# Performance work log

Hardware: AMD Instinct MI355X
Metric: run time of the kernel (lower is better)

The kernel has to match this reference:

```python
import jax, jax.numpy as jnp
import numpy as np

PNUM = 128
BATCH = 8192


def setup_inputs() -> dict:
    key = jax.random.key(0)
    k0, k1, k2 = jax.random.split(key, 3)
    return {
        "pred0": jax.random.normal(k0, (BATCH, PNUM, 2), dtype=jnp.float32),
        "pred1": jax.random.normal(k1, (BATCH, PNUM, 2), dtype=jnp.float32),
        "gt": jax.random.normal(k2, (BATCH, PNUM, 2), dtype=jnp.float32),
    }


def _smooth_l1(d):
    # F.smooth_l1_loss with default beta=1.0, reduction='none'
    a = jnp.abs(d)
    return jnp.where(a < 1.0, 0.5 * d * d, a - 0.5)


def _match_loss(pred, gt):
    # pred, gt: [B, pnum, 2]
    pnum = pred.shape[1]
    # cyclic index: idx[i, j] = (i + j) % pnum  (row i = gt rolled by i)
    idx = (jnp.arange(pnum)[:, None] + jnp.arange(pnum)[None, :]) % pnum
    gt_expand = gt[:, idx]                      # [B, pnum, pnum, 2]
    diff = pred[:, None, :, :] - gt_expand      # broadcast pred over shift dim i
    dis = _smooth_l1(diff).sum(-1).mean(axis=2)  # [B, pnum] mean over vertices j
    return jnp.min(dis, axis=1)                  # min over cyclic shift i -> [B]


def reference(pred0, pred1, gt):
    loss = _match_loss(pred0, gt).mean() + _match_loss(pred1, gt).mean()
    return loss / 2.0
```

## Files before the change

### kernel.cpp

```cpp
#include <hip/hip_runtime.h>
#include <stdint.h>

#define PNUM 128
#define BATCH 8192
#define WPB 4
#define GRID1 (BATCH / WPB)

typedef uint32_t u32;
typedef uint32_t u32x2 __attribute__((ext_vector_type(2)));
typedef uint32_t u32x4 __attribute__((ext_vector_type(4)));

__device__ __forceinline__ u32 cvt2u(float x, float y) {
    return __builtin_bit_cast(u32, __builtin_amdgcn_cvt_pkrtz(x, y));
}

#define DSR64(dst, addr) \
    asm volatile("ds_read_b64 %0, %1" : "=v"(dst) : "v"(addr))
#define DSR128(dst, addr, OFF) \
    asm volatile("ds_read_b128 %0, %1 offset:" OFF : "=v"(dst) : "v"(addr))
#define DSR2x64(dst, addr) \
    asm volatile("ds_read2_b64 %0, %1 offset0:1 offset1:2" : "=v"(dst) : "v"(addr))
#define WAITLG(N) \
    asm volatile("s_waitcnt lgkmcnt(" #N ")" ::: "memory"); \
    __builtin_amdgcn_sched_barrier(0)

#define QUAD(p0,q0,A0, p1,q1,A1, p2,q2,A2, p3,q3,A3) do { \
    u32 d0_, d1_, d2_, d3_, m0_, m1_, m2_, m3_, t0_, t1_, t2_, t3_; \
    asm volatile("v_pk_add_f16 %0, %1, %2 neg_lo:[0,1] neg_hi:[0,1]" : "=v"(d0_) : "v"(p0), "v"(q0)); \
    asm volatile("v_pk_add_f16 %0, %1, %2 neg_lo:[0,1] neg_hi:[0,1]" : "=v"(d1_) : "v"(p1), "v"(q1)); \
    asm volatile("v_pk_add_f16 %0, %1, %2 neg_lo:[0,1] neg_hi:[0,1]" : "=v"(d2_) : "v"(p2), "v"(q2)); \
    asm volatile("v_pk_add_f16 %0, %1, %2 neg_lo:[0,1] neg_hi:[0,1]" : "=v"(d3_) : "v"(p3), "v"(q3)); \
    asm volatile("v_and_b32 %0, 0x7fff7fff, %0" : "+v"(d0_)); \
    asm volatile("v_and_b32 %0, 0x7fff7fff, %0" : "+v"(d1_)); \
    asm volatile("v_and_b32 %0, 0x7fff7fff, %0" : "+v"(d2_)); \
    asm volatile("v_and_b32 %0, 0x7fff7fff, %0" : "+v"(d3_)); \
    asm volatile("v_pk_min_f16 %0, %1, %2" : "=v"(m0_) : "v"(d0_), "v"(cOne)); \
    asm volatile("v_pk_min_f16 %0, %1, %2" : "=v"(m1_) : "v"(d1_), "v"(cOne)); \
    asm volatile("v_pk_min_f16 %0, %1, %2" : "=v"(m2_) : "v"(d2_), "v"(cOne)); \
    asm volatile("v_pk_min_f16 %0, %1, %2" : "=v"(m3_) : "v"(d3_), "v"(cOne)); \
    asm volatile("v_pk_fma_f16 %0, %1, %2, %3" : "=v"(t0_) : "v"(m0_), "v"(cNegHalf), "v"(d0_)); \
    asm volatile("v_pk_fma_f16 %0, %1, %2, %3" : "=v"(t1_) : "v"(m1_), "v"(cNegHalf), "v"(d1_)); \
    asm volatile("v_pk_fma_f16 %0, %1, %2, %3" : "=v"(t2_) : "v"(m2_), "v"(cNegHalf), "v"(d2_)); \
    asm volatile("v_pk_fma_f16 %0, %1, %2, %3" : "=v"(t3_) : "v"(m3_), "v"(cNegHalf), "v"(d3_)); \
    asm volatile("v_dot2_f32_f16 %0, %1, %2, %0" : "+v"(A0) : "v"(m0_), "v"(t0_)); \
    asm volatile("v_dot2_f32_f16 %0, %1, %2, %0" : "+v"(A1) : "v"(m1_), "v"(t1_)); \
    asm volatile("v_dot2_f32_f16 %0, %1, %2, %0" : "+v"(A2) : "v"(m2_), "v"(t2_)); \
    asm volatile("v_dot2_f32_f16 %0, %1, %2, %0" : "+v"(A3) : "v"(m3_), "v"(t3_)); \
} while (0)

#define ISSUE(Bg, Bq0, Bq1) \
    DSR2x64(Bg, issGA); \
    DSR128(Bq0, issPA, "0"); \
    DSR128(Bq1, issPA, "512"); \
    issGA += 16; issPA += 16

#define COMPUTE(G, Q0, Q1, W0, W1, DO_ISSUE) \
    QUAD(Q0[0], W0,   a00,  Q0[0], W1,   a01,  Q1[0], W0,   a10,  Q1[0], W1,   a11); \
    DO_ISSUE; \
    QUAD(Q0[1], W1,   a00,  Q0[1], G[0], a01,  Q1[1], W1,   a10,  Q1[1], G[0], a11); \
    QUAD(Q0[2], G[0], a00,  Q0[2], G[1], a01,  Q1[2], G[0], a10,  Q1[2], G[1], a11); \
    QUAD(Q0[3], G[1], a00,  Q0[3], G[2], a01,  Q1[3], G[1], a10,  Q1[3], G[2], a11)

__global__ __launch_bounds__(64 * WPB, 8) void match_fused(
        const float* __restrict__ pred0,
        const float* __restrict__ pred1,
        const float* __restrict__ gt,
        float* __restrict__ ws) {
    __shared__ __align__(16) _Float16 lds[WPB][1024];
    __shared__ float bsum[WPB];

    const int t = threadIdx.x;
    const int k = t & 63;
    const int w = __builtin_amdgcn_readfirstlane(t >> 6);
    const int b = blockIdx.x * WPB + w;

    _Float16* base = lds[w];
    uint2* ringU = (uint2*)base;
    uint2* q0s   = (uint2*)(base + 512);
    uint2* q1s   = (uint2*)(base + 768);

    const float4* gv4 = (const float4*)(gt    + (size_t)b * (PNUM * 2));
    const float4* p0v = (const float4*)(pred0 + (size_t)b * (PNUM * 2));
    const float4* p1v = (const float4*)(pred1 + (size_t)b * (PNUM * 2));
    {
        float4 g = gv4[k];
        uint2 gh = {cvt2u(g.x, g.y), cvt2u(g.z, g.w)};
        ringU[k] = gh; ringU[k + 64] = gh;
        float4 p = p0v[k];
        q0s[k] = (uint2){cvt2u(p.x, p.y), cvt2u(p.z, p.w)};
        p = p1v[k];
        q1s[k] = (uint2){cvt2u(p.x, p.y), cvt2u(p.z, p.w)};
    }

    const u32 ldsb = (u32)(uintptr_t)base;
    u32 issGA = ldsb + (u32)(k * 8);
    u32 issPA = ldsb + 1024;

    asm volatile("s_waitcnt lgkmcnt(0)" ::: "memory");
    __builtin_amdgcn_sched_barrier(0);

    const u32 cOne = 0x3C003C00u;
    const u32 cNegHalf = 0xB800B800u;

    u32x2 Wsp;
    DSR64(Wsp, issGA);
    u32x4 b0g, b0q0, b0q1, b1g, b1q0, b1q1, b2g, b2q0, b2q1;
    ISSUE(b0g, b0q0, b0q1);
    ISSUE(b1g, b1q0, b1q1);

    float a00 = 0.f, a01 = 0.f, a10 = 0.f, a11 = 0.f;

    WAITLG(3); COMPUTE(b0g, b0q0, b0q1, Wsp[0], Wsp[1], ISSUE(b2g, b2q0, b2q1));
    WAITLG(3); COMPUTE(b1g, b1q0, b1q1, b0g[2], b0g[3], ISSUE(b0g, b0q0, b0q1));
    WAITLG(3); COMPUTE(b2g, b2q0, b2q1, b1g[2], b1g[3], ISSUE(b1g, b1q0, b1q1));

#pragma unroll 1
    for (int tr = 0; tr < 9; ++tr) {
        WAITLG(3); COMPUTE(b0g, b0q0, b0q1, b2g[2], b2g[3], ISSUE(b2g, b2q0, b2q1));
        WAITLG(3); COMPUTE(b1g, b1q0, b1q1, b0g[2], b0g[3], ISSUE(b0g, b0q0, b0q1));
        WAITLG(3); COMPUTE(b2g, b2q0, b2q1, b1g[2], b1g[3], ISSUE(b1g, b1q0, b1q1));
    }
    WAITLG(3); COMPUTE(b0g, b0q0, b0q1, b2g[2], b2g[3], );
    WAITLG(0); COMPUTE(b1g, b1q0, b1q1, b0g[2], b0g[3], );

    float r0 = fminf(a00, a01);
    float r1 = fminf(a10, a11);
#pragma unroll
    for (int m = 32; m > 0; m >>= 1) {
        r0 = fminf(r0, __shfl_xor(r0, m, 64));
        r1 = fminf(r1, __shfl_xor(r1, m, 64));
    }

    if (k == 0) bsum[w] = r0 + r1;
    __syncthreads();
    if (t == 0) {
        ws[blockIdx.x] = bsum[0] + bsum[1] + bsum[2] + bsum[3];
    }
}

__global__ __launch_bounds__(256) void reduce_out(
        const float* __restrict__ ws, float* __restrict__ out) {
    const int t = threadIdx.x;
    const float4* w4 = (const float4*)ws;
    float4 v0 = w4[t];
    float4 v1 = w4[t + 256];
    float s = ((v0.x + v0.y) + (v0.z + v0.w)) + ((v1.x + v1.y) + (v1.z + v1.w));
#pragma unroll
    for (int m = 32; m > 0; m >>= 1) s += __shfl_xor(s, m, 64);
    __shared__ float acc[4];
    const int w = t >> 6;
    if ((t & 63) == 0) acc[w] = s;
    __syncthreads();
    if (t == 0)
        out[0] = (acc[0] + acc[1] + acc[2] + acc[3]) * (1.0f / (2.0f * BATCH * PNUM));
}

extern "C" void kernel_launch(void* const* d_in, const int* in_sizes, int n_in,
                              void* d_out, int out_size, void* d_ws, size_t ws_size,
                              hipStream_t stream) {
    const float* pred0 = (const float*)d_in[0];
    const float* pred1 = (const float*)d_in[1];
    const float* gt    = (const float*)d_in[2];
    float* out = (float*)d_out;
    float* ws  = (float*)d_ws;

    match_fused<<<GRID1, 64 * WPB, 0, stream>>>(pred0, pred1, gt, ws);
    reduce_out<<<1, 256, 0, stream>>>(ws, out);
}
```

Before: 110.4 us.

## Fully unroll LDS-read pipeline with 4-deep ring and immediate offsets

Replaces the 3-buffer rolling loop (unroll 1) with a fully unrolled 32-step loop over a 4-slot register ring. LDS reads use constant immediate offsets instead of incremented address registers, and the prefetch distance grows from 2 to 3 steps, with waitcnt thresholds adjusted to match. The aim is to hide LDS latency better and drop loop and address overhead. In exchange, register pressure rises, so the occupancy hint in launch_bounds drops from 8 to 6.

```diff
diff --git a/kernel.cpp b/kernel.cpp
--- a/kernel.cpp
+++ b/kernel.cpp
@@ -13,16 +13,6 @@
 __device__ __forceinline__ u32 cvt2u(float x, float y) {
     return __builtin_bit_cast(u32, __builtin_amdgcn_cvt_pkrtz(x, y));
 }
-
-#define DSR64(dst, addr) \
-    asm volatile("ds_read_b64 %0, %1" : "=v"(dst) : "v"(addr))
-#define DSR128(dst, addr, OFF) \
-    asm volatile("ds_read_b128 %0, %1 offset:" OFF : "=v"(dst) : "v"(addr))
-#define DSR2x64(dst, addr) \
-    asm volatile("ds_read2_b64 %0, %1 offset0:1 offset1:2" : "=v"(dst) : "v"(addr))
-#define WAITLG(N) \
-    asm volatile("s_waitcnt lgkmcnt(" #N ")" ::: "memory"); \
-    __builtin_amdgcn_sched_barrier(0)
 
 #define QUAD(p0,q0,A0, p1,q1,A1, p2,q2,A2, p3,q3,A3) do { \
     u32 d0_, d1_, d2_, d3_, m0_, m1_, m2_, m3_, t0_, t1_, t2_, t3_; \
@@ -48,20 +38,7 @@
     asm volatile("v_dot2_f32_f16 %0, %1, %2, %0" : "+v"(A3) : "v"(m3_), "v"(t3_)); \
 } while (0)
 
-#define ISSUE(Bg, Bq0, Bq1) \
-    DSR2x64(Bg, issGA); \
-    DSR128(Bq0, issPA, "0"); \
-    DSR128(Bq1, issPA, "512"); \
-    issGA += 16; issPA += 16
-
-#define COMPUTE(G, Q0, Q1, W0, W1, DO_ISSUE) \
-    QUAD(Q0[0], W0,   a00,  Q0[0], W1,   a01,  Q1[0], W0,   a10,  Q1[0], W1,   a11); \
-    DO_ISSUE; \
-    QUAD(Q0[1], W1,   a00,  Q0[1], G[0], a01,  Q1[1], W1,   a10,  Q1[1], G[0], a11); \
-    QUAD(Q0[2], G[0], a00,  Q0[2], G[1], a01,  Q1[2], G[0], a10,  Q1[2], G[1], a11); \
-    QUAD(Q0[3], G[1], a00,  Q0[3], G[2], a01,  Q1[3], G[1], a10,  Q1[3], G[2], a11)
-
-__global__ __launch_bounds__(64 * WPB, 8) void match_fused(
+__global__ __launch_bounds__(64 * WPB, 6) void match_fused(
         const float* __restrict__ pred0,
         const float* __restrict__ pred1,
         const float* __restrict__ gt,
@@ -93,8 +70,8 @@
     }
 
     const u32 ldsb = (u32)(uintptr_t)base;
-    u32 issGA = ldsb + (u32)(k * 8);
-    u32 issPA = ldsb + 1024;
+    u32 gA = ldsb + (u32)(k * 8);
+    u32 pA = ldsb;
 
     asm volatile("s_waitcnt lgkmcnt(0)" ::: "memory");
     __builtin_amdgcn_sched_barrier(0);
@@ -103,25 +80,50 @@
     const u32 cNegHalf = 0xB800B800u;
 
     u32x2 Wsp;
-    DSR64(Wsp, issGA);
-    u32x4 b0g, b0q0, b0q1, b1g, b1q0, b1q1, b2g, b2q0, b2q1;
-    ISSUE(b0g, b0q0, b0q1);
-    ISSUE(b1g, b1q0, b1q1);
+    asm volatile("ds_read_b64 %0, %1" : "=v"(Wsp) : "v"(gA));
+    u32x4 G[4], Q0[4], Q1[4];
+#pragma unroll
+    for (int h = 0; h < 3; ++h) {
+        asm volatile("ds_read2_b64 %0, %1 offset0:%c2 offset1:%c3"
+                     : "=v"(G[h]) : "v"(gA), "i"(2 * h + 1), "i"(2 * h + 2));
+        asm volatile("ds_read_b128 %0, %1 offset:%c2"
+                     : "=v"(Q0[h]) : "v"(pA), "i"(1024 + 16 * h));
+        asm volatile("ds_read_b128 %0, %1 offset:%c2"
+                     : "=v"(Q1[h]) : "v"(pA), "i"(1536 + 16 * h));
+    }
 
     float a00 = 0.f, a01 = 0.f, a10 = 0.f, a11 = 0.f;
 
-    WAITLG(3); COMPUTE(b0g, b0q0, b0q1, Wsp[0], Wsp[1], ISSUE(b2g, b2q0, b2q1));
-    WAITLG(3); COMPUTE(b1g, b1q0, b1q1, b0g[2], b0g[3], ISSUE(b0g, b0q0, b0q1));
-    WAITLG(3); COMPUTE(b2g, b2q0, b2q1, b1g[2], b1g[3], ISSUE(b1g, b1q0, b1q1));
+#pragma unroll
+    for (int h = 0; h < 32; ++h) {
+        const int cur = h & 3;
+        const int prv = (h + 3) & 3;
+        asm volatile("s_waitcnt lgkmcnt(%c0)"
+                     :: "i"(h == 31 ? 0 : (h == 30 ? 3 : 6)) : "memory");
+        __builtin_amdgcn_sched_barrier(0);
 
-#pragma unroll 1
-    for (int tr = 0; tr < 9; ++tr) {
-        WAITLG(3); COMPUTE(b0g, b0q0, b0q1, b2g[2], b2g[3], ISSUE(b2g, b2q0, b2q1));
-        WAITLG(3); COMPUTE(b1g, b1q0, b1q1, b0g[2], b0g[3], ISSUE(b0g, b0q0, b0q1));
-        WAITLG(3); COMPUTE(b2g, b2q0, b2q1, b1g[2], b1g[3], ISSUE(b1g, b1q0, b1q1));
+        const u32 W0 = (h == 0) ? Wsp[0] : G[prv][2];
+        const u32 W1 = (h == 0) ? Wsp[1] : G[prv][3];
+
+        QUAD(Q0[cur][0], W0, a00,  Q0[cur][0], W1,        a01,
+             Q1[cur][0], W0, a10,  Q1[cur][0], W1,        a11);
+        QUAD(Q0[cur][1], W1, a00,  Q0[cur][1], G[cur][0], a01,
+             Q1[cur][1], W1, a10,  Q1[cur][1], G[cur][0], a11);
+
+        if (h < 29) {
+            asm volatile("ds_read2_b64 %0, %1 offset0:%c2 offset1:%c3"
+                         : "=v"(G[prv]) : "v"(gA), "i"(2 * (h + 3) + 1), "i"(2 * (h + 3) + 2));
+            asm volatile("ds_read_b128 %0, %1 offset:%c2"
+                         : "=v"(Q0[prv]) : "v"(pA), "i"(1024 + 16 * (h + 3)));
+            asm volatile("ds_read_b128 %0, %1 offset:%c2"
+                         : "=v"(Q1[prv]) : "v"(pA), "i"(1536 + 16 * (h + 3)));
+        }
+
+        QUAD(Q0[cur][2], G[cur][0], a00,  Q0[cur][2], G[cur][1], a01,
+             Q1[cur][2], G[cur][0], a10,  Q1[cur][2], G[cur][1], a11);
+        QUAD(Q0[cur][3], G[cur][1], a00,  Q0[cur][3], G[cur][2], a01,
+             Q1[cur][3], G[cur][1], a10,  Q1[cur][3], G[cur][2], a11);
     }
-    WAITLG(3); COMPUTE(b0g, b0q0, b0q1, b2g[2], b2g[3], );
-    WAITLG(0); COMPUTE(b1g, b1q0, b1q1, b0g[2], b0g[3], );
 
     float r0 = fminf(a00, a01);
     float r1 = fminf(a10, a11);
```

After: 108.6 us. No clear change (-1.7%).
